# Optimization experiments

Measured on AMD Instinct MI355X. Metric: run time of the kernel, lower is better.

Reference implementation:

```python
import jax, jax.numpy as jnp
import numpy as np

B, N, M, K, S, P, H, W = 8, 32, 32, 3, 1, 1, 192, 192
NH = (H + 2 * P - K) // S + 1
NW = (W + 2 * P - K) // S + 1


def setup_inputs() -> dict:
    key = jax.random.key(0)
    ks = jax.random.split(key, 8)
    f = lambda k, sh, sc: jax.random.normal(k, sh, jnp.float32) * sc
    return {
        "x": f(ks[0], (B, N, H, W), 1.0),
        "a1_w": f(ks[1], (K * K, N, K, K), 0.05),  # attention1 conv k x k
        "a1_b": jnp.zeros((K * K,), jnp.float32),
        "a2_w": f(ks[2], (K * K, K * K), 0.1),      # attention1 1x1 conv
        "a2_b": jnp.zeros((K * K,), jnp.float32),
        "a3_w": f(ks[3], (K * K, K * K), 0.1),      # attention1 1x1 conv
        "a3_b": jnp.zeros((K * K,), jnp.float32),
        "b1_w": f(ks[4], (M, N), 0.05),             # attention3 1x1 conv
        "b1_b": jnp.zeros((M,), jnp.float32),
        "b2_w": f(ks[5], (M, M), 0.05),             # attention3 1x1 conv
        "b2_b": jnp.zeros((M,), jnp.float32),
        "weight": f(ks[6], (M, N, K, K), 0.05),     # main conv weight
    }


def _attention1(x, a1_w, a1_b, a2_w, a2_b, a3_w, a3_b):
    # Conv(k) -> ReLU -> Conv1x1 -> ReLU -> Conv1x1 -> Sigmoid; out [B, K*K, NH, NW]
    a = jax.lax.conv_general_dilated(
        x, a1_w, (S, S), [(P, P), (P, P)],
        dimension_numbers=("NCHW", "OIHW", "NCHW"))
    a = jax.nn.relu(a + a1_b[None, :, None, None])
    a = jax.nn.relu(jnp.einsum("oi,bihw->bohw", a2_w, a) + a2_b[None, :, None, None])
    a = jnp.einsum("oi,bihw->bohw", a3_w, a) + a3_b[None, :, None, None]
    return jax.nn.sigmoid(a)


def _unfold(x):
    # torch F.unfold ordering: channel-major, kernel positions inner.
    # returns [B, N, K*K, NH, NW]
    xp = jnp.pad(x, ((0, 0), (0, 0), (P, P), (P, P)))
    cols = [xp[:, :, i:i + (NH - 1) * S + 1:S, j:j + (NW - 1) * S + 1:S]
            for i in range(K) for j in range(K)]
    return jnp.stack(cols, axis=2)


def reference(x, a1_w, a1_b, a2_w, a2_b, a3_w, a3_b, b1_w, b1_b, b2_w, b2_b, weight):
    att = _attention1(x, a1_w, a1_b, a2_w, a2_b, a3_w, a3_b)  # [B, K*K, NH, NW]
    pat = _unfold(x)                                          # [B, N, K*K, NH, NW]
    w = weight.reshape(M, N, K * K)
    # attention-weighted unfold + matmul + fold, fused as one einsum
    y = jnp.einsum("bnphw,bphw,mnp->bmhw", pat, att, w)       # [B, M, NH, NW]
    # attention3 bias: global avg pool -> 1x1 -> ReLU -> 1x1
    pooled = x.mean(axis=(2, 3))                              # [B, N]
    h = jax.nn.relu(pooled @ b1_w.T + b1_b)
    bias = h @ b2_w.T + b2_b                                  # [B, M]
    return y + bias[:, :, None, None]
```

## Files before the change

kernel.cpp:

```cpp
#include <hip/hip_runtime.h>
#include <math.h>

#define B_ 8
#define N_ 32
#define M_ 32
#define HW 192

typedef __attribute__((ext_vector_type(8))) short short8;
typedef __attribute__((ext_vector_type(4))) float float4_;

__device__ inline unsigned short f2bf(float f) {
    unsigned int b = __float_as_uint(f);
    b += 0x7FFF + ((b >> 16) & 1);
    return (unsigned short)(b >> 16);
}
__device__ inline float bf2f(unsigned short u) {
    return __uint_as_float((unsigned int)u << 16);
}

union U8 { short8 s; unsigned int u[4]; };

__global__ __launch_bounds__(256) void pool_prep_kernel(
    const float* __restrict__ x, const float* __restrict__ a1w,
    const float* __restrict__ weight, float* __restrict__ pooled,
    unsigned short* __restrict__ a1A, unsigned short* __restrict__ wA) {
    if (blockIdx.x == 256) {
        int tid = threadIdx.x;
        for (int idx = tid; idx < 9 * 512; idx += 256) {
            int j = idx & 7, l = (idx >> 3) & 63, c = idx >> 9;
            int o = l & 15, n = (l >> 4) * 8 + j;
            float v = (o < 9) ? a1w[(o * N_ + n) * 9 + c] : 0.f;
            a1A[idx] = f2bf(v);
        }
        for (int idx = tid; idx < 9 * 1024; idx += 256) {
            int j = idx & 7, l = (idx >> 3) & 63, mt = (idx >> 9) & 1, c = idx >> 10;
            int m = mt * 16 + (l & 15), n = (l >> 4) * 8 + j;
            wA[idx] = f2bf(weight[(m * N_ + n) * 9 + c]);
        }
        return;
    }
    int bn = blockIdx.x;
    const float4_* p = (const float4_*)(x + (size_t)bn * (HW * HW));
    float s = 0.f;
    for (int i = threadIdx.x; i < (HW * HW) / 4; i += 256) {
        float4_ v = p[i];
        s += (v[0] + v[1]) + (v[2] + v[3]);
    }
#pragma unroll
    for (int off = 32; off > 0; off >>= 1) s += __shfl_down(s, off, 64);
    __shared__ float red[4];
    if ((threadIdx.x & 63) == 0) red[threadIdx.x >> 6] = s;
    __syncthreads();
    if (threadIdx.x == 0)
        pooled[bn] = (red[0] + red[1] + red[2] + red[3]) * (1.f / (HW * HW));
}

__global__ __launch_bounds__(256, 5) void laconv_kernel(
    const float* __restrict__ x, const float* __restrict__ a1b,
    const float* __restrict__ a2w, const float* __restrict__ a2b,
    const float* __restrict__ a3w, const float* __restrict__ a3b,
    const unsigned short* __restrict__ a1A, const unsigned short* __restrict__ wA,
    const float* __restrict__ pooled, const float* __restrict__ b1w,
    const float* __restrict__ b1b, const float* __restrict__ b2w,
    const float* __restrict__ b2b, float* __restrict__ out) {
    __shared__ __align__(16) unsigned short xs[324 * 40];
    __shared__ unsigned short att_s[9 * 264];
    __shared__ float hsh[M_];
    __shared__ __align__(16) float bias_lds[M_];

    const int b = blockIdx.z;
    const int th0 = blockIdx.y * 16, tw0 = blockIdx.x * 16;
    const int tid = threadIdx.x;
    const int wv = tid >> 6, lane = tid & 63;
    const int tx = lane & 15, ks = lane >> 4;
    const float* xb = x + (size_t)b * N_ * HW * HW;

#pragma unroll
    for (int it0 = 0; it0 < 6; ++it0) {
        int it = tid + it0 * 256;
        if (it < 324 * 4) {
            int grp = it / 324;
            int pos = it - grp * 324;
            int r = pos / 18, cc = pos - r * 18;
            int h = th0 + r - 1, wc = tw0 + cc - 1;
            bool in = ((unsigned)h < HW) && ((unsigned)wc < HW);
            const float* src = xb + (size_t)(grp * 8) * (HW * HW) + h * HW + wc;
            U8 t;
#pragma unroll
            for (int i = 0; i < 4; ++i) {
                float f0 = in ? src[(2 * i) * (HW * HW)] : 0.f;
                float f1 = in ? src[(2 * i + 1) * (HW * HW)] : 0.f;
                t.u[i] = (unsigned)f2bf(f0) | ((unsigned)f2bf(f1) << 16);
            }
            *(short8*)&xs[pos * 40 + grp * 8] = t.s;
        }
    }
    if (tid < M_) {
        float s = b1b[tid];
#pragma unroll
        for (int n = 0; n < N_; n++) s += pooled[b * N_ + n] * b1w[tid * N_ + n];
        hsh[tid] = fmaxf(s, 0.f);
    }
    __syncthreads();
    if (tid < M_) {
        float s2 = b2b[tid];
#pragma unroll
        for (int q = 0; q < M_; q++) s2 += hsh[q] * b2w[tid * M_ + q];
        bias_lds[tid] = s2;
    }

    const int pb = (wv * 4) * 720 + tx * 40 + ks * 8;
    const float4_ zero4 = {0.f, 0.f, 0.f, 0.f};

    float4_ aacc[4];
#pragma unroll
    for (int g = 0; g < 4; ++g) aacc[g] = zero4;
#pragma unroll
    for (int c = 0; c < 9; ++c) {
        short8 aA = ((const short8*)a1A)[c * 64 + lane];
        const int coff = (c / 3) * 720 + (c % 3) * 40;
#pragma unroll
        for (int g = 0; g < 4; ++g) {
            short8 bP = *(const short8*)&xs[pb + g * 720 + coff];
            aacc[g] = __builtin_amdgcn_mfma_f32_16x16x32_bf16(aA, bP, aacc[g], 0, 0, 0);
        }
    }
#pragma unroll
    for (int g = 0; g < 4; ++g) {
#pragma unroll
        for (int reg = 0; reg < 4; ++reg) {
            int o = ks * 4 + reg;
            if (o < 9) att_s[o * 264 + (wv * 4 + g) * 16 + tx] = f2bf(aacc[g][reg]);
        }
    }
    __syncthreads();

    float t1[9], t2[9], attv[9];
#pragma unroll
    for (int o = 0; o < 9; ++o)
        t1[o] = fmaxf(bf2f(att_s[o * 264 + tid]) + a1b[o], 0.f);
#pragma unroll
    for (int o2 = 0; o2 < 9; ++o2) {
        float s = a2b[o2];
#pragma unroll
        for (int o = 0; o < 9; ++o) s += a2w[o2 * 9 + o] * t1[o];
        t2[o2] = fmaxf(s, 0.f);
    }
#pragma unroll
    for (int o3 = 0; o3 < 9; ++o3) {
        float s = a3b[o3];
#pragma unroll
        for (int o2 = 0; o2 < 9; ++o2) s += a3w[o3 * 9 + o2] * t2[o2];
        attv[o3] = 1.f / (1.f + __expf(-s));
    }
    __syncthreads();
#pragma unroll
    for (int p = 0; p < 9; ++p) att_s[p * 264 + tid] = f2bf(attv[p]);
    __syncthreads();

    float4_ acc0[4], acc1[4];
#pragma unroll
    for (int g = 0; g < 4; ++g) { acc0[g] = zero4; acc1[g] = zero4; }
#pragma unroll
    for (int c = 0; c < 9; ++c) {
        short8 w0 = ((const short8*)wA)[c * 128 + lane];
        short8 w1 = ((const short8*)wA)[c * 128 + 64 + lane];
        const int coff = (c / 3) * 720 + (c % 3) * 40;
#pragma unroll
        for (int g = 0; g < 4; ++g) {
            short8 bP = *(const short8*)&xs[pb + g * 720 + coff];
            float av = bf2f(att_s[c * 264 + (wv * 4 + g) * 16 + tx]);
            float4_ av4 = {av, av, av, av};
            float4_ z0 = __builtin_amdgcn_mfma_f32_16x16x32_bf16(w0, bP, zero4, 0, 0, 0);
            float4_ z1 = __builtin_amdgcn_mfma_f32_16x16x32_bf16(w1, bP, zero4, 0, 0, 0);
            acc0[g] = acc0[g] + av4 * z0;
            acc1[g] = acc1[g] + av4 * z1;
        }
    }

    const int wc = tw0 + tx;
    float4_ bv0 = *(const float4_*)&bias_lds[ks * 4];
    float4_ bv1 = *(const float4_*)&bias_lds[16 + ks * 4];
#pragma unroll
    for (int g = 0; g < 4; ++g) {
        int h = th0 + wv * 4 + g;
#pragma unroll
        for (int reg = 0; reg < 4; ++reg) {
            int m0 = ks * 4 + reg;
            out[((b * M_ + m0) * HW + h) * HW + wc] = acc0[g][reg] + bv0[reg];
            out[((b * M_ + m0 + 16) * HW + h) * HW + wc] = acc1[g][reg] + bv1[reg];
        }
    }
}

extern "C" void kernel_launch(void* const* d_in, const int* in_sizes, int n_in,
                              void* d_out, int out_size, void* d_ws,
                              size_t ws_size, hipStream_t stream) {
    const float* x   = (const float*)d_in[0];
    const float* a1w = (const float*)d_in[1];
    const float* a1b = (const float*)d_in[2];
    const float* a2w = (const float*)d_in[3];
    const float* a2b = (const float*)d_in[4];
    const float* a3w = (const float*)d_in[5];
    const float* a3b = (const float*)d_in[6];
    const float* b1w = (const float*)d_in[7];
    const float* b1b = (const float*)d_in[8];
    const float* b2w = (const float*)d_in[9];
    const float* b2b = (const float*)d_in[10];
    const float* wgt = (const float*)d_in[11];
    float* out = (float*)d_out;

    char* ws = (char*)d_ws;
    float* pooled        = (float*)(ws);
    unsigned short* a1A  = (unsigned short*)(ws + 2048);
    unsigned short* wAf  = (unsigned short*)(ws + 11264);

    pool_prep_kernel<<<dim3(B_ * N_ + 1), dim3(256), 0, stream>>>(
        x, a1w, wgt, pooled, a1A, wAf);
    laconv_kernel<<<dim3(12, 12, B_), dim3(256), 0, stream>>>(
        x, a1b, a2w, a2b, a3w, a3b, a1A, wAf, pooled, b1w, b1b, b2w, b2b, out);
    (void)in_sizes; (void)n_in; (void)out_size; (void)ws_size;
}
```

Measured before the change: 158.0 us.

## Batch halo global loads before bf16 packing, remap grid, drop redundant barrier

The halo staging loop now issues all 40 strided global loads per thread into registers first, plus a small remainder handled by 16 threads. Only then does it convert to bf16 and store to LDS, which raises memory-level parallelism in the load phase. The grid becomes 1D with the batch index in the low bits, so neighbouring blocks work on different images. A __syncthreads is removed because each thread rewrites only the att_s entries it read itself. The occupancy hint of 5 blocks per CU in launch_bounds is dropped, so the compiler may use more registers to hold the loaded values, at the risk of lower occupancy.

```diff
diff --git a/kernel.cpp b/kernel.cpp
--- a/kernel.cpp
+++ b/kernel.cpp
@@ -55,7 +55,7 @@
         pooled[bn] = (red[0] + red[1] + red[2] + red[3]) * (1.f / (HW * HW));
 }
 
-__global__ __launch_bounds__(256, 5) void laconv_kernel(
+__global__ __launch_bounds__(256) void laconv_kernel(
     const float* __restrict__ x, const float* __restrict__ a1b,
     const float* __restrict__ a2w, const float* __restrict__ a2b,
     const float* __restrict__ a3w, const float* __restrict__ a3b,
@@ -68,32 +68,67 @@
     __shared__ float hsh[M_];
     __shared__ __align__(16) float bias_lds[M_];
 
-    const int b = blockIdx.z;
-    const int th0 = blockIdx.y * 16, tw0 = blockIdx.x * 16;
+    const int id = blockIdx.x;
+    const int b = id & 7;
+    const int t = id >> 3;
+    const int bx = t % 12, by = t / 12;
+    const int th0 = by * 16, tw0 = bx * 16;
     const int tid = threadIdx.x;
     const int wv = tid >> 6, lane = tid & 63;
     const int tx = lane & 15, ks = lane >> 4;
     const float* xb = x + (size_t)b * N_ * HW * HW;
 
-#pragma unroll
-    for (int it0 = 0; it0 < 6; ++it0) {
+    float fv[5][8];
+    int posv[5], grpv[5];
+#pragma unroll
+    for (int it0 = 0; it0 < 5; ++it0) {
         int it = tid + it0 * 256;
-        if (it < 324 * 4) {
-            int grp = it / 324;
-            int pos = it - grp * 324;
-            int r = pos / 18, cc = pos - r * 18;
-            int h = th0 + r - 1, wc = tw0 + cc - 1;
-            bool in = ((unsigned)h < HW) && ((unsigned)wc < HW);
-            const float* src = xb + (size_t)(grp * 8) * (HW * HW) + h * HW + wc;
-            U8 t;
-#pragma unroll
-            for (int i = 0; i < 4; ++i) {
-                float f0 = in ? src[(2 * i) * (HW * HW)] : 0.f;
-                float f1 = in ? src[(2 * i + 1) * (HW * HW)] : 0.f;
-                t.u[i] = (unsigned)f2bf(f0) | ((unsigned)f2bf(f1) << 16);
-            }
-            *(short8*)&xs[pos * 40 + grp * 8] = t.s;
-        }
+        int grp = it / 324;
+        int pos = it - grp * 324;
+        posv[it0] = pos; grpv[it0] = grp;
+        int r = pos / 18, cc = pos - r * 18;
+        int h = th0 + r - 1, wc = tw0 + cc - 1;
+        const float* src = xb + (size_t)(grp * 8) * (HW * HW) + h * HW + wc;
+        if (((unsigned)h < HW) && ((unsigned)wc < HW)) {
+#pragma unroll
+            for (int i = 0; i < 8; ++i) fv[it0][i] = src[i * (HW * HW)];
+        } else {
+#pragma unroll
+            for (int i = 0; i < 8; ++i) fv[it0][i] = 0.f;
+        }
+    }
+    float fr[8];
+    int posr = 0;
+    if (tid < 16) {
+        int it = 1280 + tid;
+        int pos = it - 3 * 324;
+        posr = pos;
+        int r = pos / 18, cc = pos - r * 18;
+        int h = th0 + r - 1, wc = tw0 + cc - 1;
+        const float* src = xb + (size_t)24 * (HW * HW) + h * HW + wc;
+        if (((unsigned)h < HW) && ((unsigned)wc < HW)) {
+#pragma unroll
+            for (int i = 0; i < 8; ++i) fr[i] = src[i * (HW * HW)];
+        } else {
+#pragma unroll
+            for (int i = 0; i < 8; ++i) fr[i] = 0.f;
+        }
+    }
+#pragma unroll
+    for (int it0 = 0; it0 < 5; ++it0) {
+        U8 tt;
+#pragma unroll
+        for (int i = 0; i < 4; ++i)
+            tt.u[i] = (unsigned)f2bf(fv[it0][2 * i]) |
+                      ((unsigned)f2bf(fv[it0][2 * i + 1]) << 16);
+        *(short8*)&xs[posv[it0] * 40 + grpv[it0] * 8] = tt.s;
+    }
+    if (tid < 16) {
+        U8 tt;
+#pragma unroll
+        for (int i = 0; i < 4; ++i)
+            tt.u[i] = (unsigned)f2bf(fr[2 * i]) | ((unsigned)f2bf(fr[2 * i + 1]) << 16);
+        *(short8*)&xs[posr * 40 + 24] = tt.s;
     }
     if (tid < M_) {
         float s = b1b[tid];
@@ -153,7 +188,6 @@
         for (int o2 = 0; o2 < 9; ++o2) s += a3w[o3 * 9 + o2] * t2[o2];
         attv[o3] = 1.f / (1.f + __expf(-s));
     }
-    __syncthreads();
 #pragma unroll
     for (int p = 0; p < 9; ++p) att_s[p * 264 + tid] = f2bf(attv[p]);
     __syncthreads();
@@ -217,7 +251,7 @@
 
     pool_prep_kernel<<<dim3(B_ * N_ + 1), dim3(256), 0, stream>>>(
         x, a1w, wgt, pooled, a1A, wAf);
-    laconv_kernel<<<dim3(12, 12, B_), dim3(256), 0, stream>>>(
+    laconv_kernel<<<dim3(12 * 12 * B_), dim3(256), 0, stream>>>(
         x, a1b, a2w, a2b, a3w, a3b, a1A, wAf, pooled, b1w, b1b, b2w, b2b, out);
     (void)in_sizes; (void)n_in; (void)out_size; (void)ws_size;
 }
```

Result: faster. 139.3 us (-11.8%).
